# Kernel tuning notes

Measured on AMD Instinct MI355X. Metric: run time of the kernel, lower is better.

Reference implementation:

```python
import jax, jax.numpy as jnp
import numpy as np

SCALE = 0.125  # softmax_scale = 1/sqrt(head_dim=64)


def setup_inputs() -> dict:
    key = jax.random.key(0)
    ks = jax.random.split(key, 5)
    B, H, S, D = 1, 8, 256, 64
    shp = (B, H, S, D)
    return {
        "q": jax.random.normal(ks[0], shp, dtype=jnp.float32),
        "k1": jax.random.normal(ks[1], shp, dtype=jnp.float32),
        "k2": jax.random.normal(ks[2], shp, dtype=jnp.float32),
        "v1": jax.random.normal(ks[3], shp, dtype=jnp.float32),
        "v2": jax.random.normal(ks[4], shp, dtype=jnp.float32),
    }


def reference(q, k1, k2, v1, v2):
    # Trittention: 3-way score over all (i, j) key pairs per query q.
    # s[b,h,q,i,j] = sum_d Q[q,d] * K1[i,d] * K2[j,d]  (scaled)
    B, H, S, D = q.shape
    s = jnp.einsum("bhqd,bhid,bhjd->bhqij", q, k1, k2) * SCALE  # [B,H,S,S,S]
    s_flat = s.reshape(B, H, S, S * S).astype(jnp.float32)
    m = jax.nn.logsumexp(s_flat, axis=-1)               # [B,H,S] flash-style stats
    p = jax.nn.softmax(s_flat, axis=-1).reshape(B, H, S, S, S)
    # O = sum_{i,j} P * (V1_i + V2_j)
    o = (jnp.einsum("bhqij,bhid->bhqd", p, v1)
         + jnp.einsum("bhqij,bhjd->bhqd", p, v2)).astype(q.dtype)
    return o, m
```

## Files before the change

### kernel.cpp

```cpp
#include <hip/hip_runtime.h>
#include <hip/hip_bf16.h>

typedef __attribute__((ext_vector_type(8))) short short8;
typedef __attribute__((ext_vector_type(4))) float f32x4;

static constexpr int S_ = 256;
static constexpr int D_ = 64;
static constexpr int QB = 4;
static constexpr float QSCALE = 0.125f * 1.44269504088896340736f;

__device__ __forceinline__ float bf2f(short b) {
    union { unsigned int u; float f; } x;
    x.u = ((unsigned int)(unsigned short)b) << 16;
    return x.f;
}
__device__ __forceinline__ unsigned cvt_pk_bf16(float lo, float hi) {
    unsigned r;
    asm("v_cvt_pk_bf16_f32 %0, %1, %2" : "=v"(r) : "v"(lo), "v"(hi));
    return r;
}

__global__ __launch_bounds__(256, 2) void tritt_fused(
    const float* __restrict__ qg, const float* __restrict__ k1g,
    const float* __restrict__ k2g, const float* __restrict__ v1g,
    const float* __restrict__ v2g, float* __restrict__ outg)
{
    __shared__ unsigned short sK1[S_ * D_];
    __shared__ unsigned short sK2[S_ * D_];
    __shared__ float sQ[QB * D_];
    __shared__ float sPi[QB][S_];
    __shared__ float sPj[QB][S_];

    const int tid = threadIdx.x;
    const int h  = blockIdx.x >> 6;
    const int q0 = (blockIdx.x & 63) * QB;

    const float* K1h = k1g + h * (S_ * D_);
    const float* K2h = k2g + h * (S_ * D_);

    #pragma unroll
    for (int it = 0; it < 16; ++it) {
        const int e4  = tid * 4 + it * 1024;
        const int row = e4 >> 6, d = e4 & 63;
        const int idx = row * 64 + (d ^ ((row & 7) << 3));
        const float4 a = *(const float4*)(K1h + e4);
        uint2 pa; pa.x = cvt_pk_bf16(a.x, a.y); pa.y = cvt_pk_bf16(a.z, a.w);
        *(uint2*)&sK1[idx] = pa;
        const float4 b = *(const float4*)(K2h + e4);
        uint2 pb; pb.x = cvt_pk_bf16(b.x, b.y); pb.y = cvt_pk_bf16(b.z, b.w);
        *(uint2*)&sK2[idx] = pb;
    }
    sQ[tid] = qg[(h * S_ + q0 + (tid >> 6)) * D_ + (tid & 63)] * QSCALE;
    __syncthreads();

    const int w   = tid >> 6;
    const int l   = tid & 63;
    const int g   = l >> 4;
    const int sub = l & 15;

    float qs[2][8];
    #pragma unroll
    for (int k = 0; k < 2; ++k) {
        const f32x4 a = *(const f32x4*)&sQ[w * 64 + k * 32 + g * 8];
        const f32x4 b = *(const f32x4*)&sQ[w * 64 + k * 32 + g * 8 + 4];
        qs[k][0]=a[0]; qs[k][1]=a[1]; qs[k][2]=a[2]; qs[k][3]=a[3];
        qs[k][4]=b[0]; qs[k][5]=b[1]; qs[k][6]=b[2]; qs[k][7]=b[3];
    }

    float pjreg[16];
    #pragma unroll
    for (int a = 0; a < 16; ++a) pjreg[a] = 0.f;

    #pragma unroll 2
    for (int it = 0; it < 16; ++it) {
        const int arow = it * 16 + sub;
        const int asw  = (arow & 7) << 3;
        short8 af[2];
        #pragma unroll
        for (int k = 0; k < 2; ++k) {
            const short8 kf = *(const short8*)&sK1[arow * 64 + ((k * 32 + g * 8) ^ asw)];
            unsigned p0 = cvt_pk_bf16(bf2f(kf[0]) * qs[k][0], bf2f(kf[1]) * qs[k][1]);
            unsigned p1 = cvt_pk_bf16(bf2f(kf[2]) * qs[k][2], bf2f(kf[3]) * qs[k][3]);
            unsigned p2 = cvt_pk_bf16(bf2f(kf[4]) * qs[k][4], bf2f(kf[5]) * qs[k][5]);
            unsigned p3 = cvt_pk_bf16(bf2f(kf[6]) * qs[k][6], bf2f(kf[7]) * qs[k][7]);
            union { unsigned u[4]; short8 s; } pk;
            pk.u[0] = p0; pk.u[1] = p1; pk.u[2] = p2; pk.u[3] = p3;
            af[k] = pk.s;
        }

        float pireg[4] = {0.f, 0.f, 0.f, 0.f};

        #pragma unroll
        for (int jc = 0; jc < 4; ++jc) {
            f32x4 acc[4];
            #pragma unroll
            for (int jt = 0; jt < 4; ++jt) acc[jt] = (f32x4){0.f, 0.f, 0.f, 0.f};
            #pragma unroll
            for (int jt = 0; jt < 4; ++jt) {
                const int jrow = jc * 64 + jt * 16 + sub;
                const int jsw  = (jrow & 7) << 3;
                const short8 b0 = *(const short8*)&sK2[jrow * 64 + ((g * 8) ^ jsw)];
                const short8 b1 = *(const short8*)&sK2[jrow * 64 + ((32 + g * 8) ^ jsw)];
                acc[jt] = __builtin_amdgcn_mfma_f32_16x16x32_bf16(af[0], b0, acc[jt], 0, 0, 0);
                acc[jt] = __builtin_amdgcn_mfma_f32_16x16x32_bf16(af[1], b1, acc[jt], 0, 0, 0);
            }
            #pragma unroll
            for (int jt = 0; jt < 4; ++jt)
                #pragma unroll
                for (int r = 0; r < 4; ++r) {
                    const float e = __builtin_amdgcn_exp2f(acc[jt][r]);
                    pireg[r]           += e;
                    pjreg[jc * 4 + jt] += e;
                }
        }

        #pragma unroll
        for (int r = 0; r < 4; ++r) {
            float v = pireg[r];
            v += __shfl_xor(v, 1); v += __shfl_xor(v, 2);
            v += __shfl_xor(v, 4); v += __shfl_xor(v, 8);
            if (sub == 0) sPi[w][it * 16 + g * 4 + r] = v;
        }
    }

    #pragma unroll
    for (int jt = 0; jt < 16; ++jt) {
        float v = pjreg[jt];
        v += __shfl_xor(v, 16); v += __shfl_xor(v, 32);
        if (l < 16) sPj[w][jt * 16 + l] = v;
    }

    float ls = sPi[w][l] + sPi[w][64 + l] + sPi[w][128 + l] + sPi[w][192 + l];
    ls += __shfl_xor(ls, 1);  ls += __shfl_xor(ls, 2);  ls += __shfl_xor(ls, 4);
    ls += __shfl_xor(ls, 8);  ls += __shfl_xor(ls, 16); ls += __shfl_xor(ls, 32);

    const float* V1h = v1g + h * (S_ * D_);
    const float* V2h = v2g + h * (S_ * D_);
    float o = 0.f;
    #pragma unroll 4
    for (int ib = 0; ib < 32; ++ib) {
        const f32x4 a0 = *(const f32x4*)&sPi[w][ib * 8];
        const f32x4 a1 = *(const f32x4*)&sPi[w][ib * 8 + 4];
        const f32x4 b0 = *(const f32x4*)&sPj[w][ib * 8];
        const f32x4 b1 = *(const f32x4*)&sPj[w][ib * 8 + 4];
        #pragma unroll
        for (int e = 0; e < 4; ++e) {
            o += a0[e] * V1h[(ib * 8 + e) * D_ + l]     + b0[e] * V2h[(ib * 8 + e) * D_ + l];
            o += a1[e] * V1h[(ib * 8 + 4 + e) * D_ + l] + b1[e] * V2h[(ib * 8 + 4 + e) * D_ + l];
        }
    }
    outg[(h * S_ + q0 + w) * D_ + l] = o / ls;
    if (l == 0)
        outg[8 * S_ * D_ + h * S_ + q0 + w] = logf(ls);
}

extern "C" void kernel_launch(void* const* d_in, const int* in_sizes, int n_in,
                              void* d_out, int out_size, void* d_ws, size_t ws_size,
                              hipStream_t stream) {
    const float* q  = (const float*)d_in[0];
    const float* k1 = (const float*)d_in[1];
    const float* k2 = (const float*)d_in[2];
    const float* v1 = (const float*)d_in[3];
    const float* v2 = (const float*)d_in[4];
    float* out = (float*)d_out;
    tritt_fused<<<dim3(8 * (S_ / QB)), dim3(256), 0, stream>>>(q, k1, k2, v1, v2, out);
}
```

Baseline: 46.40 us.

## Split key2 dimension across blocks and add a combine kernel

Splits the j (K2) range into two halves, one per block, which doubles the grid. Each block writes a partial output and a partial sum of exponentials to workspace, and a second kernel adds the two halves, normalises, and writes the log-sum. K1 is no longer staged in LDS: each wave reads its rows straight from global memory as fp32 and scales them by q. The MFMA loop now reuses each K2 fragment across four K1 tiles, and the launch-bounds occupancy target rises from 2 to 4 blocks per CU. The aim is more parallelism and lower LDS use, paid for by an extra launch, workspace traffic, and repeated global reads of K1 by every wave.

```diff
diff --git a/kernel.cpp b/kernel.cpp
--- a/kernel.cpp
+++ b/kernel.cpp
@@ -7,51 +7,47 @@
 static constexpr int S_ = 256;
 static constexpr int D_ = 64;
 static constexpr int QB = 4;
+static constexpr int JS = 2;
+static constexpr int JH = S_ / JS;
 static constexpr float QSCALE = 0.125f * 1.44269504088896340736f;
-
-__device__ __forceinline__ float bf2f(short b) {
-    union { unsigned int u; float f; } x;
-    x.u = ((unsigned int)(unsigned short)b) << 16;
-    return x.f;
-}
+static constexpr int NBLK = 8 * (S_ / QB) * JS;
+static constexpr int WS_O_CNT = NBLK * QB * D_;
+
 __device__ __forceinline__ unsigned cvt_pk_bf16(float lo, float hi) {
     unsigned r;
     asm("v_cvt_pk_bf16_f32 %0, %1, %2" : "=v"(r) : "v"(lo), "v"(hi));
     return r;
 }
 
-__global__ __launch_bounds__(256, 2) void tritt_fused(
+__global__ __launch_bounds__(256, 4) void tritt_part(
     const float* __restrict__ qg, const float* __restrict__ k1g,
     const float* __restrict__ k2g, const float* __restrict__ v1g,
-    const float* __restrict__ v2g, float* __restrict__ outg)
+    const float* __restrict__ v2g, float* __restrict__ ws)
 {
-    __shared__ unsigned short sK1[S_ * D_];
-    __shared__ unsigned short sK2[S_ * D_];
-    __shared__ float sQ[QB * D_];
+    __shared__ unsigned short sK2[JH * D_];
     __shared__ float sPi[QB][S_];
-    __shared__ float sPj[QB][S_];
+    __shared__ float sPj[QB][JH];
 
     const int tid = threadIdx.x;
-    const int h  = blockIdx.x >> 6;
-    const int q0 = (blockIdx.x & 63) * QB;
+    const int bid = blockIdx.x;
+    const int js = bid & 1;
+    const int qt = (bid >> 1) & 63;
+    const int h  = bid >> 7;
+    const int j0 = js * JH;
+    const int q0 = qt * QB;
 
     const float* K1h = k1g + h * (S_ * D_);
     const float* K2h = k2g + h * (S_ * D_);
 
     #pragma unroll
-    for (int it = 0; it < 16; ++it) {
-        const int e4  = tid * 4 + it * 1024;
-        const int row = e4 >> 6, d = e4 & 63;
-        const int idx = row * 64 + (d ^ ((row & 7) << 3));
-        const float4 a = *(const float4*)(K1h + e4);
-        uint2 pa; pa.x = cvt_pk_bf16(a.x, a.y); pa.y = cvt_pk_bf16(a.z, a.w);
-        *(uint2*)&sK1[idx] = pa;
-        const float4 b = *(const float4*)(K2h + e4);
+    for (int it = 0; it < 8; ++it) {
+        const int e4   = tid * 4 + it * 1024;
+        const int lrow = e4 >> 6, d = e4 & 63;
+        const int idx  = lrow * 64 + (d ^ ((lrow & 7) << 3));
+        const float4 b = *(const float4*)(K2h + j0 * 64 + e4);
         uint2 pb; pb.x = cvt_pk_bf16(b.x, b.y); pb.y = cvt_pk_bf16(b.z, b.w);
         *(uint2*)&sK2[idx] = pb;
     }
-    sQ[tid] = qg[(h * S_ + q0 + (tid >> 6)) * D_ + (tid & 63)] * QSCALE;
-    __syncthreads();
 
     const int w   = tid >> 6;
     const int l   = tid & 63;
@@ -59,75 +55,88 @@
     const int sub = l & 15;
 
     float qs[2][8];
+    {
+        const float* Qrow = qg + (h * S_ + q0 + w) * D_;
+        #pragma unroll
+        for (int k = 0; k < 2; ++k) {
+            const f32x4 a = *(const f32x4*)(Qrow + k * 32 + g * 8);
+            const f32x4 b = *(const f32x4*)(Qrow + k * 32 + g * 8 + 4);
+            qs[k][0]=a[0]*QSCALE; qs[k][1]=a[1]*QSCALE; qs[k][2]=a[2]*QSCALE; qs[k][3]=a[3]*QSCALE;
+            qs[k][4]=b[0]*QSCALE; qs[k][5]=b[1]*QSCALE; qs[k][6]=b[2]*QSCALE; qs[k][7]=b[3]*QSCALE;
+        }
+    }
+    __syncthreads();
+
+    float pjreg[8];
     #pragma unroll
-    for (int k = 0; k < 2; ++k) {
-        const f32x4 a = *(const f32x4*)&sQ[w * 64 + k * 32 + g * 8];
-        const f32x4 b = *(const f32x4*)&sQ[w * 64 + k * 32 + g * 8 + 4];
-        qs[k][0]=a[0]; qs[k][1]=a[1]; qs[k][2]=a[2]; qs[k][3]=a[3];
-        qs[k][4]=b[0]; qs[k][5]=b[1]; qs[k][6]=b[2]; qs[k][7]=b[3];
-    }
-
-    float pjreg[16];
-    #pragma unroll
-    for (int a = 0; a < 16; ++a) pjreg[a] = 0.f;
-
-    #pragma unroll 2
-    for (int it = 0; it < 16; ++it) {
-        const int arow = it * 16 + sub;
-        const int asw  = (arow & 7) << 3;
-        short8 af[2];
-        #pragma unroll
-        for (int k = 0; k < 2; ++k) {
-            const short8 kf = *(const short8*)&sK1[arow * 64 + ((k * 32 + g * 8) ^ asw)];
-            unsigned p0 = cvt_pk_bf16(bf2f(kf[0]) * qs[k][0], bf2f(kf[1]) * qs[k][1]);
-            unsigned p1 = cvt_pk_bf16(bf2f(kf[2]) * qs[k][2], bf2f(kf[3]) * qs[k][3]);
-            unsigned p2 = cvt_pk_bf16(bf2f(kf[4]) * qs[k][4], bf2f(kf[5]) * qs[k][5]);
-            unsigned p3 = cvt_pk_bf16(bf2f(kf[6]) * qs[k][6], bf2f(kf[7]) * qs[k][7]);
-            union { unsigned u[4]; short8 s; } pk;
-            pk.u[0] = p0; pk.u[1] = p1; pk.u[2] = p2; pk.u[3] = p3;
-            af[k] = pk.s;
-        }
-
-        float pireg[4] = {0.f, 0.f, 0.f, 0.f};
-
-        #pragma unroll
-        for (int jc = 0; jc < 4; ++jc) {
-            f32x4 acc[4];
-            #pragma unroll
-            for (int jt = 0; jt < 4; ++jt) acc[jt] = (f32x4){0.f, 0.f, 0.f, 0.f};
+    for (int a = 0; a < 8; ++a) pjreg[a] = 0.f;
+
+    for (int pass = 0; pass < 4; ++pass) {
+        short8 af[4][2];
+        #pragma unroll
+        for (int t = 0; t < 4; ++t) {
+            const int arow = pass * 64 + t * 16 + sub;
+            #pragma unroll
+            for (int k = 0; k < 2; ++k) {
+                const f32x4 a = *(const f32x4*)(K1h + arow * 64 + k * 32 + g * 8);
+                const f32x4 b = *(const f32x4*)(K1h + arow * 64 + k * 32 + g * 8 + 4);
+                union { unsigned u[4]; short8 s; } pk;
+                pk.u[0] = cvt_pk_bf16(a[0] * qs[k][0], a[1] * qs[k][1]);
+                pk.u[1] = cvt_pk_bf16(a[2] * qs[k][2], a[3] * qs[k][3]);
+                pk.u[2] = cvt_pk_bf16(b[0] * qs[k][4], b[1] * qs[k][5]);
+                pk.u[3] = cvt_pk_bf16(b[2] * qs[k][6], b[3] * qs[k][7]);
+                af[t][k] = pk.s;
+            }
+        }
+
+        float pireg[4][4];
+        #pragma unroll
+        for (int t = 0; t < 4; ++t)
+            #pragma unroll
+            for (int r = 0; r < 4; ++r) pireg[t][r] = 0.f;
+
+        #pragma unroll
+        for (int jc = 0; jc < 2; ++jc) {
             #pragma unroll
             for (int jt = 0; jt < 4; ++jt) {
                 const int jrow = jc * 64 + jt * 16 + sub;
                 const int jsw  = (jrow & 7) << 3;
                 const short8 b0 = *(const short8*)&sK2[jrow * 64 + ((g * 8) ^ jsw)];
                 const short8 b1 = *(const short8*)&sK2[jrow * 64 + ((32 + g * 8) ^ jsw)];
-                acc[jt] = __builtin_amdgcn_mfma_f32_16x16x32_bf16(af[0], b0, acc[jt], 0, 0, 0);
-                acc[jt] = __builtin_amdgcn_mfma_f32_16x16x32_bf16(af[1], b1, acc[jt], 0, 0, 0);
+                f32x4 acc[4];
+                #pragma unroll
+                for (int t = 0; t < 4; ++t)
+                    acc[t] = __builtin_amdgcn_mfma_f32_16x16x32_bf16(af[t][0], b0, (f32x4){0.f,0.f,0.f,0.f}, 0, 0, 0);
+                #pragma unroll
+                for (int t = 0; t < 4; ++t)
+                    acc[t] = __builtin_amdgcn_mfma_f32_16x16x32_bf16(af[t][1], b1, acc[t], 0, 0, 0);
+                #pragma unroll
+                for (int t = 0; t < 4; ++t)
+                    #pragma unroll
+                    for (int r = 0; r < 4; ++r) {
+                        const float e = __builtin_amdgcn_exp2f(acc[t][r]);
+                        pireg[t][r]       += e;
+                        pjreg[jc * 4 + jt] += e;
+                    }
             }
-            #pragma unroll
-            for (int jt = 0; jt < 4; ++jt)
-                #pragma unroll
-                for (int r = 0; r < 4; ++r) {
-                    const float e = __builtin_amdgcn_exp2f(acc[jt][r]);
-                    pireg[r]           += e;
-                    pjreg[jc * 4 + jt] += e;
-                }
-        }
-
-        #pragma unroll
-        for (int r = 0; r < 4; ++r) {
-            float v = pireg[r];
-            v += __shfl_xor(v, 1); v += __shfl_xor(v, 2);
-            v += __shfl_xor(v, 4); v += __shfl_xor(v, 8);
-            if (sub == 0) sPi[w][it * 16 + g * 4 + r] = v;
-        }
+        }
+
+        #pragma unroll
+        for (int t = 0; t < 4; ++t)
+            #pragma unroll
+            for (int r = 0; r < 4; ++r) {
+                float v = pireg[t][r];
+                v += __shfl_xor(v, 1); v += __shfl_xor(v, 2);
+                v += __shfl_xor(v, 4); v += __shfl_xor(v, 8);
+                if (sub == 0) sPi[w][pass * 64 + t * 16 + g * 4 + r] = v;
+            }
     }
 
     #pragma unroll
-    for (int jt = 0; jt < 16; ++jt) {
-        float v = pjreg[jt];
+    for (int jj = 0; jj < 8; ++jj) {
+        float v = pjreg[jj];
         v += __shfl_xor(v, 16); v += __shfl_xor(v, 32);
-        if (l < 16) sPj[w][jt * 16 + l] = v;
+        if (l < 16) sPj[w][jj * 16 + l] = v;
     }
 
     float ls = sPi[w][l] + sPi[w][64 + l] + sPi[w][128 + l] + sPi[w][192 + l];
@@ -141,17 +150,42 @@
     for (int ib = 0; ib < 32; ++ib) {
         const f32x4 a0 = *(const f32x4*)&sPi[w][ib * 8];
         const f32x4 a1 = *(const f32x4*)&sPi[w][ib * 8 + 4];
+        #pragma unroll
+        for (int e = 0; e < 4; ++e) {
+            o += a0[e] * V1h[(ib * 8 + e) * D_ + l];
+            o += a1[e] * V1h[(ib * 8 + 4 + e) * D_ + l];
+        }
+    }
+    #pragma unroll 4
+    for (int ib = 0; ib < 16; ++ib) {
         const f32x4 b0 = *(const f32x4*)&sPj[w][ib * 8];
         const f32x4 b1 = *(const f32x4*)&sPj[w][ib * 8 + 4];
         #pragma unroll
         for (int e = 0; e < 4; ++e) {
-            o += a0[e] * V1h[(ib * 8 + e) * D_ + l]     + b0[e] * V2h[(ib * 8 + e) * D_ + l];
-            o += a1[e] * V1h[(ib * 8 + 4 + e) * D_ + l] + b1[e] * V2h[(ib * 8 + 4 + e) * D_ + l];
-        }
-    }
-    outg[(h * S_ + q0 + w) * D_ + l] = o / ls;
-    if (l == 0)
-        outg[8 * S_ * D_ + h * S_ + q0 + w] = logf(ls);
+            o += b0[e] * V2h[(j0 + ib * 8 + e) * D_ + l];
+            o += b1[e] * V2h[(j0 + ib * 8 + 4 + e) * D_ + l];
+        }
+    }
+    ws[(bid * QB + w) * D_ + l] = o;
+    if (l == 0) ws[WS_O_CNT + bid * QB + w] = ls;
+}
+
+__global__ __launch_bounds__(256) void tritt_combine(
+    const float* __restrict__ ws, float* __restrict__ outg)
+{
+    const int flat = blockIdx.x * 256 + threadIdx.x;
+    const int d  = flat & 63;
+    const int q  = (flat >> 6) & 3;
+    const int qt = (flat >> 8) & 63;
+    const int h  = flat >> 14;
+    const int bidA = (h * 64 + qt) * 2;
+    const int ia = (bidA) * QB + q;
+    const int ib = (bidA + 1) * QB + q;
+    const float oA = ws[ia * D_ + d], oB = ws[ib * D_ + d];
+    const float lsum = ws[WS_O_CNT + ia] + ws[WS_O_CNT + ib];
+    outg[(h * S_ + qt * QB + q) * D_ + d] = (oA + oB) / lsum;
+    if (d == 0)
+        outg[8 * S_ * D_ + h * S_ + qt * QB + q] = logf(lsum);
 }
 
 extern "C" void kernel_launch(void* const* d_in, const int* in_sizes, int n_in,
@@ -163,5 +197,7 @@
     const float* v1 = (const float*)d_in[3];
     const float* v2 = (const float*)d_in[4];
     float* out = (float*)d_out;
-    tritt_fused<<<dim3(8 * (S_ / QB)), dim3(256), 0, stream>>>(q, k1, k2, v1, v2, out);
-}
+    float* ws  = (float*)d_ws;
+    tritt_part<<<dim3(NBLK), dim3(256), 0, stream>>>(q, k1, k2, v1, v2, ws);
+    tritt_combine<<<dim3((8 * S_ * D_) / 256), dim3(256), 0, stream>>>(ws, out);
+}
```

After: 151.1 us. 3.26x slower.

## Reuse K2 fragments across four K1 tiles and split V reduction across waves

Applied to the files above, without the earlier changes.

The score loop now processes four 16-row K1 tiles per pass, so each K2 fragment read from LDS feeds four MFMAs instead of one. This cuts LDS traffic and makes the exp/row-sum accumulation more independent, at the cost of more registers. The epilogue also changes: each wave reduces a quarter of the V rows for all four queries, the partial results are combined through shared memory, and each V element is read from global memory once per block instead of four times. This adds two block-wide barriers and a shared-memory scratch buffer.

```diff
diff --git a/kernel.cpp b/kernel.cpp
--- a/kernel.cpp
+++ b/kernel.cpp
@@ -30,6 +30,8 @@
     __shared__ float sQ[QB * D_];
     __shared__ float sPi[QB][S_];
     __shared__ float sPj[QB][S_];
+    __shared__ float sTmp[4][QB * D_];
+    __shared__ float sL[QB];
 
     const int tid = threadIdx.x;
     const int h  = blockIdx.x >> 6;
@@ -71,87 +73,125 @@
     #pragma unroll
     for (int a = 0; a < 16; ++a) pjreg[a] = 0.f;
 
-    #pragma unroll 2
-    for (int it = 0; it < 16; ++it) {
-        const int arow = it * 16 + sub;
-        const int asw  = (arow & 7) << 3;
-        short8 af[2];
-        #pragma unroll
-        for (int k = 0; k < 2; ++k) {
-            const short8 kf = *(const short8*)&sK1[arow * 64 + ((k * 32 + g * 8) ^ asw)];
-            unsigned p0 = cvt_pk_bf16(bf2f(kf[0]) * qs[k][0], bf2f(kf[1]) * qs[k][1]);
-            unsigned p1 = cvt_pk_bf16(bf2f(kf[2]) * qs[k][2], bf2f(kf[3]) * qs[k][3]);
-            unsigned p2 = cvt_pk_bf16(bf2f(kf[4]) * qs[k][4], bf2f(kf[5]) * qs[k][5]);
-            unsigned p3 = cvt_pk_bf16(bf2f(kf[6]) * qs[k][6], bf2f(kf[7]) * qs[k][7]);
-            union { unsigned u[4]; short8 s; } pk;
-            pk.u[0] = p0; pk.u[1] = p1; pk.u[2] = p2; pk.u[3] = p3;
-            af[k] = pk.s;
+    for (int pass = 0; pass < 4; ++pass) {
+        short8 af[4][2];
+        #pragma unroll
+        for (int t = 0; t < 4; ++t) {
+            const int arow = pass * 64 + t * 16 + sub;
+            const int asw  = (arow & 7) << 3;
+            #pragma unroll
+            for (int k = 0; k < 2; ++k) {
+                const short8 kf = *(const short8*)&sK1[arow * 64 + ((k * 32 + g * 8) ^ asw)];
+                union { unsigned u[4]; short8 s; } pk;
+                pk.u[0] = cvt_pk_bf16(bf2f(kf[0]) * qs[k][0], bf2f(kf[1]) * qs[k][1]);
+                pk.u[1] = cvt_pk_bf16(bf2f(kf[2]) * qs[k][2], bf2f(kf[3]) * qs[k][3]);
+                pk.u[2] = cvt_pk_bf16(bf2f(kf[4]) * qs[k][4], bf2f(kf[5]) * qs[k][5]);
+                pk.u[3] = cvt_pk_bf16(bf2f(kf[6]) * qs[k][6], bf2f(kf[7]) * qs[k][7]);
+                af[t][k] = pk.s;
+            }
         }
 
-        float pireg[4] = {0.f, 0.f, 0.f, 0.f};
+        float pireg[4][4];
+        #pragma unroll
+        for (int t = 0; t < 4; ++t)
+            #pragma unroll
+            for (int r = 0; r < 4; ++r) pireg[t][r] = 0.f;
 
         #pragma unroll
         for (int jc = 0; jc < 4; ++jc) {
-            f32x4 acc[4];
-            #pragma unroll
-            for (int jt = 0; jt < 4; ++jt) acc[jt] = (f32x4){0.f, 0.f, 0.f, 0.f};
             #pragma unroll
             for (int jt = 0; jt < 4; ++jt) {
                 const int jrow = jc * 64 + jt * 16 + sub;
                 const int jsw  = (jrow & 7) << 3;
                 const short8 b0 = *(const short8*)&sK2[jrow * 64 + ((g * 8) ^ jsw)];
                 const short8 b1 = *(const short8*)&sK2[jrow * 64 + ((32 + g * 8) ^ jsw)];
-                acc[jt] = __builtin_amdgcn_mfma_f32_16x16x32_bf16(af[0], b0, acc[jt], 0, 0, 0);
-                acc[jt] = __builtin_amdgcn_mfma_f32_16x16x32_bf16(af[1], b1, acc[jt], 0, 0, 0);
-            }
-            #pragma unroll
-            for (int jt = 0; jt < 4; ++jt)
+                f32x4 acc[4];
                 #pragma unroll
-                for (int r = 0; r < 4; ++r) {
-                    const float e = __builtin_amdgcn_exp2f(acc[jt][r]);
-                    pireg[r]           += e;
-                    pjreg[jc * 4 + jt] += e;
-                }
+                for (int t = 0; t < 4; ++t)
+                    acc[t] = __builtin_amdgcn_mfma_f32_16x16x32_bf16(af[t][0], b0, (f32x4){0.f,0.f,0.f,0.f}, 0, 0, 0);
+                #pragma unroll
+                for (int t = 0; t < 4; ++t)
+                    acc[t] = __builtin_amdgcn_mfma_f32_16x16x32_bf16(af[t][1], b1, acc[t], 0, 0, 0);
+                float e[4][4];
+                #pragma unroll
+                for (int t = 0; t < 4; ++t)
+                    #pragma unroll
+                    for (int r = 0; r < 4; ++r) {
+                        e[t][r] = __builtin_amdgcn_exp2f(acc[t][r]);
+                        pireg[t][r] += e[t][r];
+                    }
+                const float s01 = (e[0][0] + e[0][1]) + (e[0][2] + e[0][3]);
+                const float s23 = (e[1][0] + e[1][1]) + (e[1][2] + e[1][3]);
+                const float s45 = (e[2][0] + e[2][1]) + (e[2][2] + e[2][3]);
+                const float s67 = (e[3][0] + e[3][1]) + (e[3][2] + e[3][3]);
+                pjreg[jc * 4 + jt] += (s01 + s23) + (s45 + s67);
+            }
         }
 
         #pragma unroll
-        for (int r = 0; r < 4; ++r) {
-            float v = pireg[r];
-            v += __shfl_xor(v, 1); v += __shfl_xor(v, 2);
-            v += __shfl_xor(v, 4); v += __shfl_xor(v, 8);
-            if (sub == 0) sPi[w][it * 16 + g * 4 + r] = v;
+        for (int t = 0; t < 4; ++t)
+            #pragma unroll
+            for (int r = 0; r < 4; ++r) {
+                float v = pireg[t][r];
+                v += __shfl_xor(v, 1); v += __shfl_xor(v, 2);
+                v += __shfl_xor(v, 4); v += __shfl_xor(v, 8);
+                if (sub == 0) sPi[w][pass * 64 + t * 16 + g * 4 + r] = v;
+            }
+    }
+
+    #pragma unroll
+    for (int jj = 0; jj < 16; ++jj) {
+        float v = pjreg[jj];
+        v += __shfl_xor(v, 16); v += __shfl_xor(v, 32);
+        if (l < 16) sPj[w][jj * 16 + l] = v;
+    }
+
+    {
+        float ls = sPi[w][l] + sPi[w][64 + l] + sPi[w][128 + l] + sPi[w][192 + l];
+        ls += __shfl_xor(ls, 1);  ls += __shfl_xor(ls, 2);  ls += __shfl_xor(ls, 4);
+        ls += __shfl_xor(ls, 8);  ls += __shfl_xor(ls, 16); ls += __shfl_xor(ls, 32);
+        if (l == 0) sL[w] = ls;
+    }
+    __syncthreads();
+
+    {
+        const int d = l;
+        const float* V1h = v1g + h * (S_ * D_);
+        const float* V2h = v2g + h * (S_ * D_);
+        float p0 = 0.f, p1 = 0.f, p2 = 0.f, p3 = 0.f;
+        #pragma unroll 4
+        for (int rb = 0; rb < 16; ++rb) {
+            const int r0 = w * 64 + rb * 4;
+            f32x4 pi0 = *(const f32x4*)&sPi[0][r0];
+            f32x4 pi1 = *(const f32x4*)&sPi[1][r0];
+            f32x4 pi2 = *(const f32x4*)&sPi[2][r0];
+            f32x4 pi3 = *(const f32x4*)&sPi[3][r0];
+            f32x4 pj0 = *(const f32x4*)&sPj[0][r0];
+            f32x4 pj1 = *(const f32x4*)&sPj[1][r0];
+            f32x4 pj2 = *(const f32x4*)&sPj[2][r0];
+            f32x4 pj3 = *(const f32x4*)&sPj[3][r0];
+            #pragma unroll
+            for (int e = 0; e < 4; ++e) {
+                const float v1 = V1h[(r0 + e) * D_ + d];
+                const float v2 = V2h[(r0 + e) * D_ + d];
+                p0 += pi0[e] * v1 + pj0[e] * v2;
+                p1 += pi1[e] * v1 + pj1[e] * v2;
+                p2 += pi2[e] * v1 + pj2[e] * v2;
+                p3 += pi3[e] * v1 + pj3[e] * v2;
+            }
         }
-    }
-
-    #pragma unroll
-    for (int jt = 0; jt < 16; ++jt) {
-        float v = pjreg[jt];
-        v += __shfl_xor(v, 16); v += __shfl_xor(v, 32);
-        if (l < 16) sPj[w][jt * 16 + l] = v;
-    }
-
-    float ls = sPi[w][l] + sPi[w][64 + l] + sPi[w][128 + l] + sPi[w][192 + l];
-    ls += __shfl_xor(ls, 1);  ls += __shfl_xor(ls, 2);  ls += __shfl_xor(ls, 4);
-    ls += __shfl_xor(ls, 8);  ls += __shfl_xor(ls, 16); ls += __shfl_xor(ls, 32);
-
-    const float* V1h = v1g + h * (S_ * D_);
-    const float* V2h = v2g + h * (S_ * D_);
-    float o = 0.f;
-    #pragma unroll 4
-    for (int ib = 0; ib < 32; ++ib) {
-        const f32x4 a0 = *(const f32x4*)&sPi[w][ib * 8];
-        const f32x4 a1 = *(const f32x4*)&sPi[w][ib * 8 + 4];
-        const f32x4 b0 = *(const f32x4*)&sPj[w][ib * 8];
-        const f32x4 b1 = *(const f32x4*)&sPj[w][ib * 8 + 4];
-        #pragma unroll
-        for (int e = 0; e < 4; ++e) {
-            o += a0[e] * V1h[(ib * 8 + e) * D_ + l]     + b0[e] * V2h[(ib * 8 + e) * D_ + l];
-            o += a1[e] * V1h[(ib * 8 + 4 + e) * D_ + l] + b1[e] * V2h[(ib * 8 + 4 + e) * D_ + l];
-        }
-    }
-    outg[(h * S_ + q0 + w) * D_ + l] = o / ls;
-    if (l == 0)
-        outg[8 * S_ * D_ + h * S_ + q0 + w] = logf(ls);
+        sTmp[w][0 * 64 + d] = p0; sTmp[w][1 * 64 + d] = p1;
+        sTmp[w][2 * 64 + d] = p2; sTmp[w][3 * 64 + d] = p3;
+    }
+    __syncthreads();
+    {
+        const int q = tid >> 6, d = tid & 63;
+        const float oo = sTmp[0][q * 64 + d] + sTmp[1][q * 64 + d]
+                       + sTmp[2][q * 64 + d] + sTmp[3][q * 64 + d];
+        outg[(h * S_ + q0 + q) * D_ + d] = oo / sL[q];
+        if (tid < QB)
+            outg[8 * S_ * D_ + h * S_ + q0 + tid] = logf(sL[tid]);
+    }
 }
 
 extern "C" void kernel_launch(void* const* d_in, const int* in_sizes, int n_in,
```

Result: slower. 128.2 us (+176.3%).
